# Performance work log

Measured on AMD Instinct MI355X. Metric: run time of the kernel, lower is better.

The kernel has to match this reference:

```python
import jax, jax.numpy as jnp
import numpy as np

T, D, I, E, G, LG, K = 2048, 1024, 512, 32, 8, 4, 6
SI = 2 * I  # shared expert inter dim = n_shared_experts * inter_dim
ROUTE_SCALE = 1.0


def setup_inputs() -> dict:
    key = jax.random.key(0)
    ks = jax.random.split(key, 16)
    s = 0.02
    f = jnp.float32
    return {
        "x": jax.random.normal(ks[0], (T, D), f),
        "router_w": jax.random.normal(ks[1], (E, D), f) * s,
        "router_b": jax.random.normal(ks[2], (E,), f) * s,
        "W1": jax.random.normal(ks[3], (E, D, I), f) * s,
        "b1": jax.random.normal(ks[4], (E, I), f) * s,
        "W2": jax.random.normal(ks[5], (E, D, I), f) * s,
        "b2": jax.random.normal(ks[6], (E, I), f) * s,
        "W3": jax.random.normal(ks[7], (E, I, D), f) * s,
        "b3": jax.random.normal(ks[8], (E, D), f) * s,
        "sw1": jax.random.normal(ks[9], (D, SI), f) * s,
        "sb1": jax.random.normal(ks[10], (SI,), f) * s,
        "sw2": jax.random.normal(ks[11], (D, SI), f) * s,
        "sb2": jax.random.normal(ks[12], (SI,), f) * s,
        "sw3": jax.random.normal(ks[13], (SI, D), f) * s,
        "sb3": jax.random.normal(ks[14], (D,), f) * s,
    }


def _route(x, router_w, router_b):
    # Router: softmax scores (fp32), group-limited top-k.
    logits = x @ router_w.T + router_b                      # [T, E]
    scores = jax.nn.softmax(logits.astype(jnp.float32), axis=-1)
    original = scores
    sg = scores.reshape(x.shape[0], G, E // G)              # [T, G, E/G]
    # no router bias -> group score = sum of top-2 expert scores per group
    group_scores = jnp.sum(jax.lax.top_k(sg, 2)[0], axis=-1)  # [T, G]
    _, gidx = jax.lax.top_k(group_scores, LG)               # [T, LG]
    keep = jnp.zeros((x.shape[0], G), bool).at[jnp.arange(x.shape[0])[:, None], gidx].set(True)
    masked = jnp.where(keep[:, :, None], sg, -jnp.inf).reshape(x.shape[0], E)
    _, idx = jax.lax.top_k(masked, K)                       # [T, K]
    vals = jnp.take_along_axis(original, idx, axis=1) * ROUTE_SCALE
    return vals.astype(x.dtype), idx


def reference(x, router_w, router_b, W1, b1, W2, b2, W3, b3, sw1, sb1, sw2, sb2, sw3, sb3):
    vals, idx = _route(x, router_w, router_b)
    # dense gate matrix [T, E]; top-k indices per row are distinct
    gates = jnp.zeros((x.shape[0], E), x.dtype).at[jnp.arange(x.shape[0])[:, None], idx].set(vals)
    # routed experts: Expert(x) = W3 @ silu(w1(x) * w2(x))
    h1 = jnp.einsum('td,edi->tei', x, W1) + b1              # [T, E, I]
    h2 = jnp.einsum('td,edi->tei', x, W2) + b2
    h = jax.nn.silu(h1 * h2)
    y = jnp.einsum('tei,eid->td', h * gates[:, :, None], W3) + gates @ b3
    # shared expert
    z = jax.nn.silu((x @ sw1 + sb1) * (x @ sw2 + sb2)) @ sw3 + sb3
    return y + z
```

## Files before the change

### kernel.cpp

```cpp
#include <hip/hip_runtime.h>
#include <hip/hip_bf16.h>
#include <math.h>

#define T_CONST 2048
#define D_CONST 1024
#define I_CONST 512
#define SI_CONST 1024
#define E_CONST 32
#define G_CONST 8
#define LG_CONST 4
#define KSEL 6
#define BK 32

typedef __attribute__((ext_vector_type(8))) short short8;
typedef __attribute__((ext_vector_type(4))) float floatx4;

__device__ inline unsigned pack_bf16(float a, float b) {
  __hip_bfloat162 h = __float22bfloat162_rn(float2{a, b});
  return *reinterpret_cast<unsigned*>(&h);
}

__device__ inline void gload16(const void* g, void* l) {
  __builtin_amdgcn_global_load_lds(
      (const __attribute__((address_space(1))) unsigned int*)g,
      (__attribute__((address_space(3))) unsigned int*)l, 16, 0, 0);
}

__global__ __launch_bounds__(256) void prep_all(
    const float* __restrict__ x, const float* __restrict__ rw,
    const float* __restrict__ W1, const float* __restrict__ W2,
    const float* __restrict__ W3, const float* __restrict__ sw1,
    const float* __restrict__ sw2, const float* __restrict__ sw3,
    __hip_bfloat16* __restrict__ x_bf, float* __restrict__ rwt,
    __hip_bfloat16* __restrict__ W1t, __hip_bfloat16* __restrict__ W2t,
    __hip_bfloat16* __restrict__ W3t, __hip_bfloat16* __restrict__ sw1t,
    __hip_bfloat16* __restrict__ sw2t, __hip_bfloat16* __restrict__ sw3t) {
  const int b = blockIdx.x;
  const int tid = threadIdx.x;
  if (b >= 3264) {
    int lb = b - 3264;
    if (lb < 512) {
      size_t base = (size_t)lb * 4096 + tid * 4;
#pragma unroll
      for (int it = 0; it < 4; ++it) {
        float4 v = *(const float4*)&x[base + it * 1024];
        uint2 u{pack_bf16(v.x, v.y), pack_bf16(v.z, v.w)};
        *(uint2*)&x_bf[base + it * 1024] = u;
      }
    } else {
      int lb2 = lb - 512;
#pragma unroll
      for (int it = 0; it < 4; ++it) {
        int i = lb2 * 1024 + it * 256 + tid;
        int d = i >> 5, e = i & 31;
        rwt[d * 32 + e] = rw[e * D_CONST + d];
      }
    }
    return;
  }
  const float* in;
  __hip_bfloat16* out;
  int K, N, k0, n0;
  if (b < 2048) {
    int mat = b >> 5, rem = b & 31;
    K = 1024; N = 512;
    int e = mat & 31;
    in = ((mat < 32) ? W1 : W2) + (size_t)e * (1024 * 512);
    out = ((mat < 32) ? W1t : W2t) + (size_t)e * (1024 * 512);
    k0 = (rem >> 3) * 256; n0 = (rem & 7) * 64;
  } else if (b < 3072) {
    int local = b - 2048;
    int e = local >> 5, rem = local & 31;
    K = 512; N = 1024;
    in = W3 + (size_t)e * (512 * 1024);
    out = W3t + (size_t)e * (512 * 1024);
    k0 = (rem >> 4) * 256; n0 = (rem & 15) * 64;
  } else {
    int local = b - 3072;
    int which = local >> 6, rem = local & 63;
    K = 1024; N = 1024;
    in = which == 0 ? sw1 : which == 1 ? sw2 : sw3;
    out = which == 0 ? sw1t : which == 1 ? sw2t : sw3t;
    k0 = (rem >> 4) * 256; n0 = (rem & 15) * 64;
  }
  __shared__ short tile[64 * 256];
  const int u = tid & 15, tr = tid >> 4;
#pragma unroll
  for (int sub = 0; sub < 4; ++sub) {
    float4 v[4];
#pragma unroll
    for (int r = 0; r < 4; ++r)
      v[r] = *(const float4*)&in[(size_t)(k0 + sub * 64 + 4 * tr + r) * N + n0 + 4 * u];
    int kb = sub * 64 + 4 * tr;
    int chunk = kb >> 3, half = (kb >> 2) & 1;
#pragma unroll
    for (int j = 0; j < 4; ++j) {
      int n = 4 * u + j;
      unsigned lo = pack_bf16(((const float*)&v[0])[j], ((const float*)&v[1])[j]);
      unsigned hi = pack_bf16(((const float*)&v[2])[j], ((const float*)&v[3])[j]);
      int cx = chunk ^ ((n >> 2) & 7) ^ ((n & 3) << 3);
      *(uint2*)&tile[n * 256 + cx * 8 + half * 4] = uint2{lo, hi};
    }
  }
  __syncthreads();
  const int n_ = tid >> 5, c_ = tid & 31;
#pragma unroll
  for (int p = 0; p < 8; ++p) {
    int n = p * 8 + n_;
    int cx = c_ ^ ((n >> 2) & 7) ^ ((n & 3) << 3);
    uint4 o = *(const uint4*)&tile[n * 256 + cx * 8];
    *(uint4*)&out[(size_t)(n0 + n) * K + k0 + c_ * 8] = o;
  }
}

__global__ __launch_bounds__(256) void router2(
    const float* __restrict__ x, const float* __restrict__ rwt,
    const float* __restrict__ rb, int* __restrict__ counts,
    int* __restrict__ stok, float* __restrict__ gatel) {
  const int lane = threadIdx.x & 63;
  const int wv = threadIdx.x >> 6;
  const int t = blockIdx.x * 4 + wv;
  const int e = lane & 31, h = lane >> 5;
  const float* xp = x + (size_t)t * D_CONST;
  float s = 0.f;
#pragma unroll 8
  for (int d = h; d < D_CONST; d += 2) s = fmaf(xp[d], rwt[d * 32 + e], s);
  s += __shfl_xor(s, 32);
  s += rb[e];
  float mx = s;
#pragma unroll
  for (int m = 16; m >= 1; m >>= 1) mx = fmaxf(mx, __shfl_xor(mx, m));
  float p = expf(s - mx);
  float sum = p;
#pragma unroll
  for (int m = 16; m >= 1; m >>= 1) sum += __shfl_xor(sum, m);
  float sc = p / sum;
  float a = sc, bb = __shfl_xor(a, 1);
  float hi = fmaxf(a, bb), lo = fminf(a, bb);
  float oh = __shfl_xor(hi, 2), ol = __shfl_xor(lo, 2);
  float gs = fmaxf(fmaxf(hi + oh, hi + lo), oh + ol);
  const int g = e >> 2;
  unsigned keep = 0;
  float gv = gs;
#pragma unroll
  for (int r = 0; r < LG_CONST; ++r) {
    float v = gv;
    int gi = g;
#pragma unroll
    for (int m = 16; m >= 1; m >>= 1) {
      float ov = __shfl_xor(v, m);
      int og = __shfl_xor(gi, m);
      if (ov > v || (ov == v && og < gi)) { v = ov; gi = og; }
    }
    keep |= 1u << gi;
    if (g == gi) gv = -1e30f;
  }
  float cand = ((keep >> g) & 1u) ? sc : -1e30f;
  int sel_e = -1;
  float sel_v = 0.f;
#pragma unroll
  for (int r = 0; r < KSEL; ++r) {
    float v = cand;
    int ei = e;
#pragma unroll
    for (int m = 16; m >= 1; m >>= 1) {
      float ov = __shfl_xor(v, m);
      int oe = __shfl_xor(ei, m);
      if (ov > v || (ov == v && oe < ei)) { v = ov; ei = oe; }
    }
    if (lane == r) { sel_e = ei; sel_v = v; }
    if (e == ei) cand = -1e30f;
  }
  if (lane < KSEL) {
    int pos = atomicAdd(&counts[sel_e], 1);
    stok[sel_e * T_CONST + pos] = t;
    gatel[sel_e * T_CONST + pos] = sel_v;
  }
}

__global__ __launch_bounds__(64) void plan_build(
    const int* __restrict__ counts, int* __restrict__ offsets,
    int* __restrict__ plan_up, int* __restrict__ plan_dn, int* __restrict__ meta) {
  const int lane = threadIdx.x;
  for (int i = lane; i < 128; i += 64) {
    int ent = (E_CONST << 8) | i;
    plan_up[i] = ent;
    plan_dn[i] = ent;
  }
  int cnt = (lane < E_CONST) ? counts[lane] : 0;
  int incl = cnt;
#pragma unroll
  for (int d = 1; d < 64; d <<= 1) {
    int v = __shfl_up(incl, d);
    if (lane >= d) incl += v;
  }
  if (lane < E_CONST) offsets[lane] = incl - cnt;
  if (lane == E_CONST - 1) offsets[E_CONST] = incl;
  int mbs = (cnt + 127) >> 7;
  int pm = mbs;
#pragma unroll
  for (int d = 1; d < 64; d <<= 1) {
    int v = __shfl_up(pm, d);
    if (lane >= d) pm += v;
  }
  int pmex = pm - mbs;
  if (lane < E_CONST) {
    int ub = 128 + pmex * 4, db = 128 + pmex * 8;
    for (int mb = 0; mb < mbs; ++mb) {
#pragma unroll
      for (int nb = 0; nb < 4; ++nb)
        plan_up[ub + mb * 4 + nb] = (lane << 8) | (mb << 3) | nb;
#pragma unroll
      for (int nb = 0; nb < 8; ++nb)
        plan_dn[db + mb * 8 + nb] = (lane << 8) | (mb << 3) | nb;
    }
  }
  if (lane == E_CONST - 1) {
    meta[0] = 128 + pm * 4;
    meta[1] = 128 + pm * 8;
  }
}

__global__ __launch_bounds__(256) void gather_x(
    const __hip_bfloat16* __restrict__ xbf, const int* __restrict__ counts,
    const int* __restrict__ offsets, const int* __restrict__ stok,
    const float* __restrict__ gatel, __hip_bfloat16* __restrict__ Xg,
    float* __restrict__ cgate, int* __restrict__ tcnt, int* __restrict__ tslot) {
  int e = blockIdx.x;
  int cnt = counts[e];
  int row = blockIdx.y * 16 + (threadIdx.x >> 4);
  if (row >= cnt) return;
  int seg = threadIdx.x & 15;
  int tok = stok[e * T_CONST + row];
  int dst = offsets[e] + row;
  const uint4* src = (const uint4*)(xbf + (size_t)tok * D_CONST);
  uint4* d = (uint4*)(Xg + (size_t)dst * D_CONST);
#pragma unroll
  for (int i = 0; i < 8; ++i) d[i * 16 + seg] = src[i * 16 + seg];
  if (seg == 0) {
    cgate[dst] = gatel[e * T_CONST + row];
    int sl = atomicAdd(&tcnt[tok], 1);
    tslot[tok * 8 + sl] = dst;
  }
}

__global__ __launch_bounds__(512, 4) void up_fused(
    const __hip_bfloat16* __restrict__ Xg, const __hip_bfloat16* __restrict__ xbf,
    const __hip_bfloat16* __restrict__ W1t, const __hip_bfloat16* __restrict__ W2t,
    const __hip_bfloat16* __restrict__ sw1t, const __hip_bfloat16* __restrict__ sw2t,
    const float* __restrict__ b1, const float* __restrict__ b2,
    const float* __restrict__ sb1, const float* __restrict__ sb2,
    const int* __restrict__ counts, const int* __restrict__ offsets,
    const int* __restrict__ plan, const int* __restrict__ meta,
    __hip_bfloat16* __restrict__ He, __hip_bfloat16* __restrict__ Hs) {
  const int nw = meta[0];
  const int bx = blockIdx.x;
  if (bx >= nw) return;
  const int q = nw >> 3, r = nw & 7, c = bx & 7, sl = bx >> 3;
  const int j = (c < r ? c * (q + 1) : r * (q + 1) + (c - r) * q) + sl;
  const int ent = plan[j];
  const int z = ent >> 8;
  const int m0 = ((ent >> 3) & 31) * 128;
  const int n0 = (ent & 7) * 128;
  const bool SH = (z == E_CONST);
  const int cnt = SH ? T_CONST : counts[z];
  const int base = SH ? 0 : offsets[z];

  const __hip_bfloat16* Ab = SH ? (xbf + (size_t)m0 * D_CONST)
                                : (Xg + (size_t)(base + m0) * D_CONST);
  const __hip_bfloat16* B1 = SH ? (sw1t + (size_t)n0 * D_CONST)
                                : (W1t + ((size_t)z * I_CONST + n0) * D_CONST);
  const __hip_bfloat16* B2 = SH ? (sw2t + (size_t)n0 * D_CONST)
                                : (W2t + ((size_t)z * I_CONST + n0) * D_CONST);

  __shared__ short As[3 * 4096], Bs1[3 * 4096], Bs2[3 * 4096];

  const int tid = threadIdx.x, lane = tid & 63, wv = tid >> 6;
  const int l15 = lane & 15, quad = lane >> 4;
  const int wm = wv & 1, wn = wv >> 1;
  const int srow = tid >> 2;
  const int slc = tid & 3;
  const int kap = slc ^ ((srow >> 1) & 3);

  const __hip_bfloat16* aG  = Ab + (size_t)srow * D_CONST + kap * 8;
  const __hip_bfloat16* b1G = B1 + (size_t)srow * D_CONST + kap * 8;
  const __hip_bfloat16* b2G = B2 + (size_t)srow * D_CONST + kap * 8;
  const int ldsu = tid * 8;

  floatx4 acc1[4][2] = {};
  floatx4 acc2[4][2] = {};

  const int nIter = D_CONST / BK;

  auto stage = [&](int slot, int kk) {
    const int sb = slot * 4096;
    gload16(aG + kk,  &As [sb + ldsu]);
    gload16(b1G + kk, &Bs1[sb + ldsu]);
    gload16(b2G + kk, &Bs2[sb + ldsu]);
  };

  stage(0, 0);
  stage(1, BK);
  int sl0 = 0, sl1 = 1, sl2 = 2;

  for (int s = 0; s < nIter; ++s) {
    int kn = (s + 2 < nIter) ? (s + 2) * BK : (nIter - 1) * BK;
    stage(sl2, kn);
    asm volatile("s_waitcnt vmcnt(6)" ::: "memory");
    __builtin_amdgcn_s_barrier();
    const int sb = sl0 * 4096;
    short8 x1[2], x2[2];
#pragma unroll
    for (int ni = 0; ni < 2; ++ni) {
      int n = wn * 32 + ni * 16 + l15;
      int uo = sb + n * 32 + (quad ^ ((n >> 1) & 3)) * 8;
      x1[ni] = *(const short8*)&Bs1[uo];
      x2[ni] = *(const short8*)&Bs2[uo];
    }
    __builtin_amdgcn_s_setprio(1);
#pragma unroll
    for (int mi = 0; mi < 4; ++mi) {
      int m = wm * 64 + mi * 16 + l15;
      short8 a = *(const short8*)&As[sb + m * 32 + (quad ^ ((m >> 1) & 3)) * 8];
#pragma unroll
      for (int ni = 0; ni < 2; ++ni) {
        acc1[mi][ni] = __builtin_amdgcn_mfma_f32_16x16x32_bf16(a, x1[ni], acc1[mi][ni], 0, 0, 0);
        acc2[mi][ni] = __builtin_amdgcn_mfma_f32_16x16x32_bf16(a, x2[ni], acc2[mi][ni], 0, 0, 0);
      }
    }
    __builtin_amdgcn_s_setprio(0);
    __builtin_amdgcn_s_barrier();
    int t = sl0; sl0 = sl1; sl1 = sl2; sl2 = t;
  }
  asm volatile("s_waitcnt vmcnt(0)" ::: "memory");

  const float* pb1 = SH ? sb1 : (b1 + (size_t)z * I_CONST);
  const float* pb2 = SH ? sb2 : (b2 + (size_t)z * I_CONST);
  __hip_bfloat16* outp = SH ? (Hs + (size_t)m0 * SI_CONST + n0)
                            : (He + (size_t)(base + m0) * I_CONST + n0);
  const int ldo = SH ? SI_CONST : I_CONST;
  float c1[2], c2[2];
#pragma unroll
  for (int ni = 0; ni < 2; ++ni) {
    int n = wn * 32 + ni * 16 + l15;
    c1[ni] = pb1[n0 + n];
    c2[ni] = pb2[n0 + n];
  }
#pragma unroll
  for (int mi = 0; mi < 4; ++mi) {
#pragma unroll
    for (int reg = 0; reg < 4; ++reg) {
      int m = wm * 64 + mi * 16 + quad * 4 + reg;
      if (m0 + m >= cnt) continue;
#pragma unroll
      for (int ni = 0; ni < 2; ++ni) {
        int n = wn * 32 + ni * 16 + l15;
        float h1 = acc1[mi][ni][reg] + c1[ni];
        float h2 = acc2[mi][ni][reg] + c2[ni];
        float p = h1 * h2;
        float sg = p / (1.f + expf(-p));
        outp[(size_t)m * ldo + n] = __float2bfloat16(sg);
      }
    }
  }
}

__global__ __launch_bounds__(512, 4) void down_fused(
    const __hip_bfloat16* __restrict__ He, const __hip_bfloat16* __restrict__ Hs,
    const __hip_bfloat16* __restrict__ W3t, const __hip_bfloat16* __restrict__ sw3t,
    const float* __restrict__ b3, const float* __restrict__ sb3,
    const int* __restrict__ counts, const int* __restrict__ offsets,
    const float* __restrict__ cgate, const int* __restrict__ plan,
    const int* __restrict__ meta, float* __restrict__ Yp, float* __restrict__ out) {
  if ((int)blockIdx.x >= meta[1]) return;
  const int ent = plan[blockIdx.x];
  const int z = ent >> 8;
  const int m0 = ((ent >> 3) & 31) * 128;
  const int n0 = (ent & 7) * 128;
  const bool SH = (z == E_CONST);
  const int cnt = SH ? T_CONST : counts[z];
  const int base = SH ? 0 : offsets[z];
  const int Kd = SH ? SI_CONST : I_CONST;

  const __hip_bfloat16* Ab = SH ? (Hs + (size_t)m0 * SI_CONST)
                                : (He + (size_t)(base + m0) * I_CONST);
  const __hip_bfloat16* Bb = SH ? (sw3t + (size_t)n0 * SI_CONST)
                                : (W3t + ((size_t)z * D_CONST + n0) * I_CONST);

  __shared__ short As[2 * 4096], Bs[2 * 4096];

  const int tid = threadIdx.x, lane = tid & 63, wv = tid >> 6;
  const int l15 = lane & 15, quad = lane >> 4;
  const int wm = wv & 1, wn = wv >> 1;
  const int srow = tid >> 2, slc = tid & 3;
  const int kap = slc ^ ((srow >> 1) & 3);

  const __hip_bfloat16* aG = Ab + (size_t)srow * Kd + kap * 8;
  const __hip_bfloat16* bG = Bb + (size_t)srow * Kd + kap * 8;
  const int ldsu = tid * 8;

  floatx4 acc[4][2] = {};
  const int nIter = Kd / BK;

  auto stage = [&](int slot, int kk) {
    const int sb = slot * 4096;
    gload16(aG + kk, &As[sb + ldsu]);
    gload16(bG + kk, &Bs[sb + ldsu]);
  };

  stage(0, 0);
  int cur = 0;

  for (int s = 0; s < nIter; ++s) {
    int kn = (s + 1 < nIter) ? (s + 1) * BK : s * BK;
    stage(cur ^ 1, kn);
    asm volatile("s_waitcnt vmcnt(2)" ::: "memory");
    __builtin_amdgcn_s_barrier();
    const int sb = cur * 4096;
    short8 bb[2];
#pragma unroll
    for (int ni = 0; ni < 2; ++ni) {
      int n = wn * 32 + ni * 16 + l15;
      bb[ni] = *(const short8*)&Bs[sb + n * 32 + (quad ^ ((n >> 1) & 3)) * 8];
    }
    __builtin_amdgcn_s_setprio(1);
#pragma unroll
    for (int mi = 0; mi < 4; ++mi) {
      int m = wm * 64 + mi * 16 + l15;
      short8 a = *(const short8*)&As[sb + m * 32 + (quad ^ ((m >> 1) & 3)) * 8];
#pragma unroll
      for (int ni = 0; ni < 2; ++ni)
        acc[mi][ni] = __builtin_amdgcn_mfma_f32_16x16x32_bf16(a, bb[ni], acc[mi][ni], 0, 0, 0);
    }
    __builtin_amdgcn_s_setprio(0);
    __builtin_amdgcn_s_barrier();
    cur ^= 1;
  }
  asm volatile("s_waitcnt vmcnt(0)" ::: "memory");

  float bias[2];
#pragma unroll
  for (int ni = 0; ni < 2; ++ni) {
    int n = n0 + wn * 32 + ni * 16 + l15;
    bias[ni] = SH ? sb3[n] : b3[(size_t)z * D_CONST + n];
  }
#pragma unroll
  for (int mi = 0; mi < 4; ++mi) {
#pragma unroll
    for (int reg = 0; reg < 4; ++reg) {
      int m = wm * 64 + mi * 16 + quad * 4 + reg;
      if (m0 + m >= cnt) continue;
#pragma unroll
      for (int ni = 0; ni < 2; ++ni) {
        int n = n0 + wn * 32 + ni * 16 + l15;
        float v = acc[mi][ni][reg] + bias[ni];
        if (SH) {
          out[(size_t)(m0 + m) * D_CONST + n] = v;
        } else {
          int grow = base + m0 + m;
          Yp[(size_t)grow * D_CONST + n] = cgate[grow] * v;
        }
      }
    }
  }
}

__global__ __launch_bounds__(256) void combine(
    const float* __restrict__ Yp, const int* __restrict__ tslot,
    float* __restrict__ out) {
  const int t = blockIdx.x;
  const int d = threadIdx.x * 4;
  const int* ts = &tslot[t * 8];
  float4 o = *(const float4*)&out[(size_t)t * D_CONST + d];
#pragma unroll
  for (int k = 0; k < KSEL; ++k) {
    float4 y = *(const float4*)&Yp[(size_t)ts[k] * D_CONST + d];
    o.x += y.x; o.y += y.y; o.z += y.z; o.w += y.w;
  }
  *(float4*)&out[(size_t)t * D_CONST + d] = o;
}

extern "C" void kernel_launch(void* const* d_in, const int* in_sizes, int n_in,
                              void* d_out, int out_size, void* d_ws, size_t ws_size,
                              hipStream_t stream) {
  const float* x   = (const float*)d_in[0];
  const float* rw  = (const float*)d_in[1];
  const float* rb  = (const float*)d_in[2];
  const float* W1  = (const float*)d_in[3];
  const float* b1  = (const float*)d_in[4];
  const float* W2  = (const float*)d_in[5];
  const float* b2  = (const float*)d_in[6];
  const float* W3  = (const float*)d_in[7];
  const float* b3  = (const float*)d_in[8];
  const float* sw1 = (const float*)d_in[9];
  const float* sb1 = (const float*)d_in[10];
  const float* sw2 = (const float*)d_in[11];
  const float* sb2 = (const float*)d_in[12];
  const float* sw3 = (const float*)d_in[13];
  const float* sb3 = (const float*)d_in[14];
  float* out = (float*)d_out;

  char* w = (char*)d_ws;
  size_t off = 0;
  auto alloc = [&](size_t bytes) {
    char* p = w + off;
    off += (bytes + 255) & ~(size_t)255;
    return p;
  };
  int* counts = (int*)alloc(E_CONST * 4);
  int* offsets = (int*)alloc((E_CONST + 1) * 4);
  int* meta = (int*)alloc(16);
  int* plan_up = (int*)alloc(768 * 4);
  int* plan_dn = (int*)alloc(1280 * 4);
  int* tcnt = (int*)alloc((size_t)T_CONST * 4);
  int* tslot = (int*)alloc((size_t)T_CONST * 8 * 4);
  int* stok = (int*)alloc((size_t)E_CONST * T_CONST * 4);
  float* gatel = (float*)alloc((size_t)E_CONST * T_CONST * 4);
  float* rwt = (float*)alloc((size_t)D_CONST * E_CONST * 4);
  float* cgate = (float*)alloc((size_t)T_CONST * KSEL * 4);
  __hip_bfloat16* x_bf = (__hip_bfloat16*)alloc((size_t)T_CONST * D_CONST * 2);
  __hip_bfloat16* Xg = (__hip_bfloat16*)alloc((size_t)(T_CONST * KSEL + 128) * D_CONST * 2);
  __hip_bfloat16* W1t = (__hip_bfloat16*)alloc((size_t)E_CONST * D_CONST * I_CONST * 2);
  __hip_bfloat16* W2t = (__hip_bfloat16*)alloc((size_t)E_CONST * D_CONST * I_CONST * 2);
  __hip_bfloat16* W3t = (__hip_bfloat16*)alloc((size_t)E_CONST * I_CONST * D_CONST * 2);
  __hip_bfloat16* sw1t = (__hip_bfloat16*)alloc((size_t)D_CONST * SI_CONST * 2);
  __hip_bfloat16* sw2t = (__hip_bfloat16*)alloc((size_t)D_CONST * SI_CONST * 2);
  __hip_bfloat16* sw3t = (__hip_bfloat16*)alloc((size_t)SI_CONST * D_CONST * 2);
  __hip_bfloat16* He = (__hip_bfloat16*)alloc((size_t)(T_CONST * KSEL + 128) * I_CONST * 2);
  __hip_bfloat16* Hs = (__hip_bfloat16*)alloc((size_t)T_CONST * SI_CONST * 2);
  float* Yp = (float*)W1t;

  hipMemsetAsync(counts, 0, E_CONST * sizeof(int), stream);
  hipMemsetAsync(tcnt, 0, (size_t)T_CONST * sizeof(int), stream);
  prep_all<<<3808, 256, 0, stream>>>(x, rw, W1, W2, W3, sw1, sw2, sw3,
                                     x_bf, rwt, W1t, W2t, W3t, sw1t, sw2t, sw3t);
  router2<<<T_CONST / 4, 256, 0, stream>>>(x, rwt, rb, counts, stok, gatel);
  plan_build<<<1, 64, 0, stream>>>(counts, offsets, plan_up, plan_dn, meta);
  gather_x<<<dim3(E_CONST, T_CONST / 16), 256, 0, stream>>>(
      x_bf, counts, offsets, stok, gatel, Xg, cgate, tcnt, tslot);
  up_fused<<<768, 512, 0, stream>>>(
      Xg, x_bf, W1t, W2t, sw1t, sw2t, b1, b2, sb1, sb2, counts, offsets,
      plan_up, meta, He, Hs);
  down_fused<<<1280, 512, 0, stream>>>(
      He, Hs, W3t, sw3t, b3, sb3, counts, offsets, cgate, plan_dn, meta, Yp, out);
  combine<<<T_CONST, 256, 0, stream>>>(Yp, tslot, out);
}
```

Baseline: 448.9 us.

## Fuse router into prep kernel and gather expert rows indirectly in up GEMM

```diff
diff --git a/kernel.cpp b/kernel.cpp
--- a/kernel.cpp
+++ b/kernel.cpp
@@ -28,13 +28,16 @@
 
 __global__ __launch_bounds__(256) void prep_all(
     const float* __restrict__ x, const float* __restrict__ rw,
+    const float* __restrict__ rbias,
     const float* __restrict__ W1, const float* __restrict__ W2,
     const float* __restrict__ W3, const float* __restrict__ sw1,
     const float* __restrict__ sw2, const float* __restrict__ sw3,
-    __hip_bfloat16* __restrict__ x_bf, float* __restrict__ rwt,
+    __hip_bfloat16* __restrict__ x_bf,
     __hip_bfloat16* __restrict__ W1t, __hip_bfloat16* __restrict__ W2t,
     __hip_bfloat16* __restrict__ W3t, __hip_bfloat16* __restrict__ sw1t,
-    __hip_bfloat16* __restrict__ sw2t, __hip_bfloat16* __restrict__ sw3t) {
+    __hip_bfloat16* __restrict__ sw2t, __hip_bfloat16* __restrict__ sw3t,
+    int* __restrict__ counts, int* __restrict__ stok,
+    float* __restrict__ gatel) {
   const int b = blockIdx.x;
   const int tid = threadIdx.x;
   if (b >= 3264) {
@@ -48,12 +51,66 @@
         *(uint2*)&x_bf[base + it * 1024] = u;
       }
     } else {
-      int lb2 = lb - 512;
-#pragma unroll
-      for (int it = 0; it < 4; ++it) {
-        int i = lb2 * 1024 + it * 256 + tid;
-        int d = i >> 5, e = i & 31;
-        rwt[d * 32 + e] = rw[e * D_CONST + d];
+      int rblk = lb - 512;
+      const int lane = tid & 63;
+      const int wvr = tid >> 6;
+      const int t = rblk * 4 + wvr;
+      const int e = lane & 31, h = lane >> 5;
+      const float* xp = x + (size_t)t * D_CONST;
+      const float* wp = rw + (size_t)e * D_CONST;
+      float s = 0.f;
+#pragma unroll 8
+      for (int d = h; d < D_CONST; d += 2) s = fmaf(xp[d], wp[d], s);
+      s += __shfl_xor(s, 32);
+      s += rbias[e];
+      float mx = s;
+#pragma unroll
+      for (int m = 16; m >= 1; m >>= 1) mx = fmaxf(mx, __shfl_xor(mx, m));
+      float p = expf(s - mx);
+      float sum = p;
+#pragma unroll
+      for (int m = 16; m >= 1; m >>= 1) sum += __shfl_xor(sum, m);
+      float sc = p / sum;
+      float a = sc, bb2 = __shfl_xor(a, 1);
+      float hi = fmaxf(a, bb2), lo = fminf(a, bb2);
+      float oh = __shfl_xor(hi, 2), ol = __shfl_xor(lo, 2);
+      float gs = fmaxf(fmaxf(hi + oh, hi + lo), oh + ol);
+      const int g = e >> 2;
+      unsigned keep = 0;
+      float gv = gs;
+#pragma unroll
+      for (int r = 0; r < LG_CONST; ++r) {
+        float v = gv;
+        int gi = g;
+#pragma unroll
+        for (int m = 16; m >= 1; m >>= 1) {
+          float ov = __shfl_xor(v, m);
+          int og = __shfl_xor(gi, m);
+          if (ov > v || (ov == v && og < gi)) { v = ov; gi = og; }
+        }
+        keep |= 1u << gi;
+        if (g == gi) gv = -1e30f;
+      }
+      float cand = ((keep >> g) & 1u) ? sc : -1e30f;
+      int sel_e = -1;
+      float sel_v = 0.f;
+#pragma unroll
+      for (int r = 0; r < KSEL; ++r) {
+        float v = cand;
+        int ei = e;
+#pragma unroll
+        for (int m = 16; m >= 1; m >>= 1) {
+          float ov = __shfl_xor(v, m);
+          int oe = __shfl_xor(ei, m);
+          if (ov > v || (ov == v && oe < ei)) { v = ov; ei = oe; }
+        }
+        if (lane == r) { sel_e = ei; sel_v = v; }
+        if (e == ei) cand = -1e30f;
+      }
+      if (lane < KSEL) {
+        int pos = atomicAdd(&counts[sel_e], 1);
+        stok[sel_e * T_CONST + pos] = t;
+        gatel[sel_e * T_CONST + pos] = sel_v;
       }
     }
     return;
@@ -113,71 +170,6 @@
   }
 }
 
-__global__ __launch_bounds__(256) void router2(
-    const float* __restrict__ x, const float* __restrict__ rwt,
-    const float* __restrict__ rb, int* __restrict__ counts,
-    int* __restrict__ stok, float* __restrict__ gatel) {
-  const int lane = threadIdx.x & 63;
-  const int wv = threadIdx.x >> 6;
-  const int t = blockIdx.x * 4 + wv;
-  const int e = lane & 31, h = lane >> 5;
-  const float* xp = x + (size_t)t * D_CONST;
-  float s = 0.f;
-#pragma unroll 8
-  for (int d = h; d < D_CONST; d += 2) s = fmaf(xp[d], rwt[d * 32 + e], s);
-  s += __shfl_xor(s, 32);
-  s += rb[e];
-  float mx = s;
-#pragma unroll
-  for (int m = 16; m >= 1; m >>= 1) mx = fmaxf(mx, __shfl_xor(mx, m));
-  float p = expf(s - mx);
-  float sum = p;
-#pragma unroll
-  for (int m = 16; m >= 1; m >>= 1) sum += __shfl_xor(sum, m);
-  float sc = p / sum;
-  float a = sc, bb = __shfl_xor(a, 1);
-  float hi = fmaxf(a, bb), lo = fminf(a, bb);
-  float oh = __shfl_xor(hi, 2), ol = __shfl_xor(lo, 2);
-  float gs = fmaxf(fmaxf(hi + oh, hi + lo), oh + ol);
-  const int g = e >> 2;
-  unsigned keep = 0;
-  float gv = gs;
-#pragma unroll
-  for (int r = 0; r < LG_CONST; ++r) {
-    float v = gv;
-    int gi = g;
-#pragma unroll
-    for (int m = 16; m >= 1; m >>= 1) {
-      float ov = __shfl_xor(v, m);
-      int og = __shfl_xor(gi, m);
-      if (ov > v || (ov == v && og < gi)) { v = ov; gi = og; }
-    }
-    keep |= 1u << gi;
-    if (g == gi) gv = -1e30f;
-  }
-  float cand = ((keep >> g) & 1u) ? sc : -1e30f;
-  int sel_e = -1;
-  float sel_v = 0.f;
-#pragma unroll
-  for (int r = 0; r < KSEL; ++r) {
-    float v = cand;
-    int ei = e;
-#pragma unroll
-    for (int m = 16; m >= 1; m >>= 1) {
-      float ov = __shfl_xor(v, m);
-      int oe = __shfl_xor(ei, m);
-      if (ov > v || (ov == v && oe < ei)) { v = ov; ei = oe; }
-    }
-    if (lane == r) { sel_e = ei; sel_v = v; }
-    if (e == ei) cand = -1e30f;
-  }
-  if (lane < KSEL) {
-    int pos = atomicAdd(&counts[sel_e], 1);
-    stok[sel_e * T_CONST + pos] = t;
-    gatel[sel_e * T_CONST + pos] = sel_v;
-  }
-}
-
 __global__ __launch_bounds__(64) void plan_build(
     const int* __restrict__ counts, int* __restrict__ offsets,
     int* __restrict__ plan_up, int* __restrict__ plan_dn, int* __restrict__ meta) {
@@ -221,23 +213,18 @@
   }
 }
 
-__global__ __launch_bounds__(256) void gather_x(
-    const __hip_bfloat16* __restrict__ xbf, const int* __restrict__ counts,
-    const int* __restrict__ offsets, const int* __restrict__ stok,
-    const float* __restrict__ gatel, __hip_bfloat16* __restrict__ Xg,
-    float* __restrict__ cgate, int* __restrict__ tcnt, int* __restrict__ tslot) {
-  int e = blockIdx.x;
-  int cnt = counts[e];
-  int row = blockIdx.y * 16 + (threadIdx.x >> 4);
-  if (row >= cnt) return;
-  int seg = threadIdx.x & 15;
-  int tok = stok[e * T_CONST + row];
-  int dst = offsets[e] + row;
-  const uint4* src = (const uint4*)(xbf + (size_t)tok * D_CONST);
-  uint4* d = (uint4*)(Xg + (size_t)dst * D_CONST);
-#pragma unroll
-  for (int i = 0; i < 8; ++i) d[i * 16 + seg] = src[i * 16 + seg];
-  if (seg == 0) {
+__global__ __launch_bounds__(256) void gather_meta(
+    const int* __restrict__ counts, const int* __restrict__ offsets,
+    const int* __restrict__ stok, const float* __restrict__ gatel,
+    int* __restrict__ ctok, float* __restrict__ cgate,
+    int* __restrict__ tcnt, int* __restrict__ tslot) {
+  const int e = blockIdx.x;
+  const int cnt = counts[e];
+  const int base = offsets[e];
+  for (int row = threadIdx.x; row < cnt; row += 256) {
+    int tok = stok[e * T_CONST + row];
+    int dst = base + row;
+    ctok[dst] = tok;
     cgate[dst] = gatel[e * T_CONST + row];
     int sl = atomicAdd(&tcnt[tok], 1);
     tslot[tok * 8 + sl] = dst;
@@ -245,13 +232,14 @@
 }
 
 __global__ __launch_bounds__(512, 4) void up_fused(
-    const __hip_bfloat16* __restrict__ Xg, const __hip_bfloat16* __restrict__ xbf,
+    const __hip_bfloat16* __restrict__ xbf,
     const __hip_bfloat16* __restrict__ W1t, const __hip_bfloat16* __restrict__ W2t,
     const __hip_bfloat16* __restrict__ sw1t, const __hip_bfloat16* __restrict__ sw2t,
     const float* __restrict__ b1, const float* __restrict__ b2,
     const float* __restrict__ sb1, const float* __restrict__ sb2,
     const int* __restrict__ counts, const int* __restrict__ offsets,
-    const int* __restrict__ plan, const int* __restrict__ meta,
+    const int* __restrict__ ctok, const int* __restrict__ plan,
+    const int* __restrict__ meta,
     __hip_bfloat16* __restrict__ He, __hip_bfloat16* __restrict__ Hs) {
   const int nw = meta[0];
   const int bx = blockIdx.x;
@@ -266,8 +254,6 @@
   const int cnt = SH ? T_CONST : counts[z];
   const int base = SH ? 0 : offsets[z];
 
-  const __hip_bfloat16* Ab = SH ? (xbf + (size_t)m0 * D_CONST)
-                                : (Xg + (size_t)(base + m0) * D_CONST);
   const __hip_bfloat16* B1 = SH ? (sw1t + (size_t)n0 * D_CONST)
                                 : (W1t + ((size_t)z * I_CONST + n0) * D_CONST);
   const __hip_bfloat16* B2 = SH ? (sw2t + (size_t)n0 * D_CONST)
@@ -282,7 +268,9 @@
   const int slc = tid & 3;
   const int kap = slc ^ ((srow >> 1) & 3);
 
-  const __hip_bfloat16* aG  = Ab + (size_t)srow * D_CONST + kap * 8;
+  const int arow = m0 + srow;
+  const int tok = SH ? arow : ((arow < cnt) ? ctok[base + arow] : 0);
+  const __hip_bfloat16* aG  = xbf + (size_t)tok * D_CONST + kap * 8;
   const __hip_bfloat16* b1G = B1 + (size_t)srow * D_CONST + kap * 8;
   const __hip_bfloat16* b2G = B2 + (size_t)srow * D_CONST + kap * 8;
   const int ldsu = tid * 8;
@@ -516,10 +504,9 @@
   int* tslot = (int*)alloc((size_t)T_CONST * 8 * 4);
   int* stok = (int*)alloc((size_t)E_CONST * T_CONST * 4);
   float* gatel = (float*)alloc((size_t)E_CONST * T_CONST * 4);
-  float* rwt = (float*)alloc((size_t)D_CONST * E_CONST * 4);
-  float* cgate = (float*)alloc((size_t)T_CONST * KSEL * 4);
+  int* ctok = (int*)alloc((size_t)(T_CONST * KSEL + 128) * 4);
+  float* cgate = (float*)alloc((size_t)(T_CONST * KSEL + 128) * 4);
   __hip_bfloat16* x_bf = (__hip_bfloat16*)alloc((size_t)T_CONST * D_CONST * 2);
-  __hip_bfloat16* Xg = (__hip_bfloat16*)alloc((size_t)(T_CONST * KSEL + 128) * D_CONST * 2);
   __hip_bfloat16* W1t = (__hip_bfloat16*)alloc((size_t)E_CONST * D_CONST * I_CONST * 2);
   __hip_bfloat16* W2t = (__hip_bfloat16*)alloc((size_t)E_CONST * D_CONST * I_CONST * 2);
   __hip_bfloat16* W3t = (__hip_bfloat16*)alloc((size_t)E_CONST * I_CONST * D_CONST * 2);
@@ -532,15 +519,15 @@
 
   hipMemsetAsync(counts, 0, E_CONST * sizeof(int), stream);
   hipMemsetAsync(tcnt, 0, (size_t)T_CONST * sizeof(int), stream);
-  prep_all<<<3808, 256, 0, stream>>>(x, rw, W1, W2, W3, sw1, sw2, sw3,
-                                     x_bf, rwt, W1t, W2t, W3t, sw1t, sw2t, sw3t);
-  router2<<<T_CONST / 4, 256, 0, stream>>>(x, rwt, rb, counts, stok, gatel);
+  prep_all<<<4288, 256, 0, stream>>>(x, rw, rb, W1, W2, W3, sw1, sw2, sw3,
+                                     x_bf, W1t, W2t, W3t, sw1t, sw2t, sw3t,
+                                     counts, stok, gatel);
   plan_build<<<1, 64, 0, stream>>>(counts, offsets, plan_up, plan_dn, meta);
-  gather_x<<<dim3(E_CONST, T_CONST / 16), 256, 0, stream>>>(
-      x_bf, counts, offsets, stok, gatel, Xg, cgate, tcnt, tslot);
+  gather_meta<<<E_CONST, 256, 0, stream>>>(counts, offsets, stok, gatel,
+                                           ctok, cgate, tcnt, tslot);
   up_fused<<<768, 512, 0, stream>>>(
-      Xg, x_bf, W1t, W2t, sw1t, sw2t, b1, b2, sb1, sb2, counts, offsets,
-      plan_up, meta, He, Hs);
+      x_bf, W1t, W2t, sw1t, sw2t, b1, b2, sb1, sb2, counts, offsets,
+      ctok, plan_up, meta, He, Hs);
   down_fused<<<1280, 512, 0, stream>>>(
       He, Hs, W3t, sw3t, b3, sb3, counts, offsets, cgate, plan_dn, meta, Yp, out);
   combine<<<T_CONST, 256, 0, stream>>>(Yp, tslot, out);
```

Result: slower. 623.1 us (+38.8%).
